# Optimization experiments

Measured on AMD Instinct MI355X. Metric: run time of the kernel, lower is better.

Reference implementation:

```python
import jax, jax.numpy as jnp
import numpy as np

TOKENS = 8192
HIDDEN = 6144
NUM_EXPERTS = 768  # n_routed_experts (512) + zero_expert_num (256)
TOP_K = 12
ROUTED_SCALING_FACTOR = 2.5


def setup_inputs() -> dict:
    key = jax.random.key(0)
    k1, k2, k3 = jax.random.split(key, 3)
    hidden_states = jax.random.normal(k1, (TOKENS, HIDDEN), dtype=jnp.float32)
    classifier_weight = jax.random.normal(k2, (NUM_EXPERTS, HIDDEN), dtype=jnp.float32) * (1.0 / np.sqrt(HIDDEN))
    e_score_correction_bias = jax.random.normal(k3, (NUM_EXPERTS,), dtype=jnp.float32) * 0.1
    return {
        "hidden_states": hidden_states,
        "classifier_weight": classifier_weight,
        "e_score_correction_bias": e_score_correction_bias,
    }


def reference(hidden_states, classifier_weight, e_score_correction_bias):
    # [T, H] -> router logits [T, E] in fp32 (source casts to float32)
    x = hidden_states.reshape(-1, HIDDEN).astype(jnp.float32)
    router_logits = jnp.einsum('th,eh->te', x, classifier_weight)

    # npu_moe_gating_top_k(renorm=0, norm_type=0): softmax scores,
    # bias-corrected selection, gather un-biased scores, scale.
    scores = jax.nn.softmax(router_logits, axis=-1)                # [T, E]
    scores_for_choice = scores + e_score_correction_bias[None, :]  # [T, E]
    _, topk_indices = jax.lax.top_k(scores_for_choice, TOP_K)       # [T, K]
    topk_weights = jnp.take_along_axis(scores, topk_indices, axis=-1)
    topk_weights = topk_weights * ROUTED_SCALING_FACTOR

    return topk_indices.astype(jnp.int32), topk_weights
```

## Files before the change

kernel.cpp:

```cpp
#include <hip/hip_runtime.h>

#define TOKENS  8192
#define HIDDEN  6144
#define EXPERTS 768
#define TOPK    12
#define RSF     2.5f
#define ROWH    (HIDDEN * 2)

typedef float    f4 __attribute__((ext_vector_type(4)));
typedef _Float16 h8 __attribute__((ext_vector_type(8)));
typedef _Float16 h2 __attribute__((ext_vector_type(2)));
typedef __fp16   g2 __attribute__((ext_vector_type(2)));

#define BM 128
#define BN 96
#define NKT 192
#define AH   8192
#define BLO  3072
#define BUFH 14336
#define LO_SCALE 4096.0f
#define LO_INV   2.44140625e-4f

static __device__ inline h2 pk(float a, float b) {
    g2 r = __builtin_amdgcn_cvt_pkrtz(a, b);
    return __builtin_bit_cast(h2, r);
}

static __device__ inline void cvt8(const f4 a, const f4 b, h8& hi, h8& lo) {
    h2 ha = pk(a.x, a.y), hb = pk(a.z, a.w), hc = pk(b.x, b.y), hd = pk(b.z, b.w);
    h2 la = pk((a.x - (float)ha[0]) * LO_SCALE, (a.y - (float)ha[1]) * LO_SCALE);
    h2 lb = pk((a.z - (float)hb[0]) * LO_SCALE, (a.w - (float)hb[1]) * LO_SCALE);
    h2 lc = pk((b.x - (float)hc[0]) * LO_SCALE, (b.y - (float)hc[1]) * LO_SCALE);
    h2 ld = pk((b.z - (float)hd[0]) * LO_SCALE, (b.w - (float)hd[1]) * LO_SCALE);
    hi[0]=ha[0]; hi[1]=ha[1]; hi[2]=hb[0]; hi[3]=hb[1];
    hi[4]=hc[0]; hi[5]=hc[1]; hi[6]=hd[0]; hi[7]=hd[1];
    lo[0]=la[0]; lo[1]=la[1]; lo[2]=lb[0]; lo[3]=lb[1];
    lo[4]=lc[0]; lo[5]=lc[1]; lo[6]=ld[0]; lo[7]=ld[1];
}

__global__ __launch_bounds__(256)
void split_convert_w(const float* W, _Float16* WO) {
    const int row = blockIdx.x;
    const float* src = W + (size_t)row * HIDDEN;
    _Float16*   dst = WO + (size_t)row * ROWH;
    const int t = threadIdx.x;
    f4 a[3], b[3];
#pragma unroll
    for (int i = 0; i < 3; ++i) {
        const f4* p = (const f4*)(src + (size_t)(t + 256 * i) * 8);
        a[i] = p[0]; b[i] = p[1];
    }
    __syncthreads();
#pragma unroll
    for (int i = 0; i < 3; ++i) {
        h8 hi, lo;
        cvt8(a[i], b[i], hi, lo);
        const int g = t + 256 * i;
        *(h8*)(dst + (size_t)g * 8)          = hi;
        *(h8*)(dst + HIDDEN + (size_t)g * 8) = lo;
    }
}

typedef __attribute__((address_space(1))) const void av1;
typedef __attribute__((address_space(3))) void av3;
static __device__ inline void stage16(const void* g, void* l) {
    __builtin_amdgcn_global_load_lds((av1*)g, (av3*)l, 16, 0, 0);
}

__global__ __launch_bounds__(256, 2)
void router_gemm(const float* __restrict__ X, const _Float16* __restrict__ Ws,
                 float* __restrict__ L) {
    __shared__ _Float16 sm[2 * BUFH];

    const int t    = threadIdx.x;
    const int bm   = blockIdx.x * BM;
    const int bn   = blockIdx.y * BN;
    const int lane = t & 63;
    const int w    = t >> 6;
    const int lr   = lane & 15;
    const int lq   = lane >> 4;

    const float* psA[4];
    uint32_t     ldsoA[4];
#pragma unroll
    for (int q = 0; q < 4; ++q) {
        const int jA = w * 4 + q;
        const int r  = jA * 8 + (lane >> 3);
        const int p  = lane & 7;
        const int c  = p ^ (r & 7);
        psA[q]   = X + (size_t)(bm + r) * HIDDEN + c * 4;
        ldsoA[q] = (uint32_t)(jA * 512);
    }

    const _Float16* psB[3];
    uint32_t        ldsoB[3];
#pragma unroll
    for (int q = 0; q < 3; ++q) {
        const int j    = w * 3 + q;
        const int isLo = (j >= 6);
        const int jj   = isLo ? j - 6 : j;
        const int r    = jj * 16 + (lane >> 2);
        const int p    = lane & 3;
        const int g    = p ^ ((r >> 1) & 3);
        psB[q]   = Ws + (size_t)(bn + r) * ROWH + g * 8 + isLo * HIDDEN;
        ldsoB[q] = (uint32_t)(AH + isLo * BLO + jj * 512);
    }

    uint32_t aoff[4];
#pragma unroll
    for (int mi = 0; mi < 4; ++mi) {
        const int r = (w & 1) * 64 + mi * 16 + lr;
        aoff[mi] = r * 64 + (uint32_t)(((2 * lq) ^ (r & 7)) * 8);
    }
    uint32_t boff[3];
#pragma unroll
    for (int ni = 0; ni < 3; ++ni) {
        const int r = (w >> 1) * 48 + ni * 16 + lr;
        boff[ni] = AH + r * 32 + ((lq ^ ((r >> 1) & 3)) * 8);
    }

    f4 acc_h[4][3], acc_c[4][3];
#pragma unroll
    for (int i = 0; i < 4; ++i)
#pragma unroll
        for (int j = 0; j < 3; ++j) { acc_h[i][j] = f4{0,0,0,0}; acc_c[i][j] = f4{0,0,0,0}; }

#pragma unroll
    for (int q = 0; q < 4; ++q) { stage16((const void*)psA[q], (void*)(sm + ldsoA[q])); psA[q] += 32; }
#pragma unroll
    for (int q = 0; q < 3; ++q) { stage16((const void*)psB[q], (void*)(sm + ldsoB[q])); psB[q] += 32; }

    auto do_tile = [&](const uint32_t boR, const uint32_t boW, const bool doStage) {
        if (doStage) {
#pragma unroll
            for (int q = 0; q < 4; ++q) { stage16((const void*)psA[q], (void*)(sm + boW + ldsoA[q])); psA[q] += 32; }
#pragma unroll
            for (int q = 0; q < 3; ++q) { stage16((const void*)psB[q], (void*)(sm + boW + ldsoB[q])); psB[q] += 32; }
        }
        h8 ah[4], al[4], bh[3], bl[3];
#pragma unroll
        for (int mi = 0; mi < 4; ++mi) {
            const uint32_t ao = boR + aoff[mi];
            const f4 va = *(const f4*)(sm + ao);
            const f4 vb = *(const f4*)(sm + (ao ^ 8u));
            cvt8(va, vb, ah[mi], al[mi]);
        }
#pragma unroll
        for (int ni = 0; ni < 3; ++ni) {
            bh[ni] = *(const h8*)(sm + boR + boff[ni]);
            bl[ni] = *(const h8*)(sm + boR + boff[ni] + BLO);
        }
#pragma unroll
        for (int mi = 0; mi < 4; ++mi)
#pragma unroll
            for (int ni = 0; ni < 3; ++ni) {
                acc_h[mi][ni] = __builtin_amdgcn_mfma_f32_16x16x32_f16(ah[mi], bh[ni], acc_h[mi][ni], 0, 0, 0);
                acc_c[mi][ni] = __builtin_amdgcn_mfma_f32_16x16x32_f16(ah[mi], bl[ni], acc_c[mi][ni], 0, 0, 0);
                acc_c[mi][ni] = __builtin_amdgcn_mfma_f32_16x16x32_f16(al[mi], bh[ni], acc_c[mi][ni], 0, 0, 0);
            }
    };

    for (int T2 = 0; T2 < NKT / 2; ++T2) {
        __syncthreads();
        do_tile(0u, (uint32_t)BUFH, true);
        __syncthreads();
        do_tile((uint32_t)BUFH, 0u, T2 != NKT / 2 - 1);
    }

#pragma unroll
    for (int mi = 0; mi < 4; ++mi)
#pragma unroll
        for (int ni = 0; ni < 3; ++ni)
#pragma unroll
            for (int r = 0; r < 4; ++r) {
                const int gm = bm + (w & 1) * 64 + mi * 16 + lq * 4 + r;
                const int gn = bn + (w >> 1) * 48 + ni * 16 + lr;
                L[(size_t)gm * EXPERTS + gn] = acc_h[mi][ni][r] + acc_c[mi][ni][r] * LO_INV;
            }
}

__global__ __launch_bounds__(256)
void router_topk(const float* __restrict__ L, const float* __restrict__ bias,
                 float* __restrict__ outIdx, float* __restrict__ outW) {
    __shared__ float sb[EXPERTS];
    const int t = threadIdx.x;
    for (int i = t; i < EXPERTS; i += 256) sb[i] = bias[i];
    __syncthreads();

    const int lane  = t & 63;
    const int wave  = t >> 6;
    const int token = blockIdx.x * 4 + wave;
    const float* row = L + (size_t)token * EXPERTS;

    float lg[12];
#pragma unroll
    for (int j = 0; j < 12; ++j) lg[j] = row[lane + 64 * j];

    float m = lg[0];
#pragma unroll
    for (int j = 1; j < 12; ++j) m = fmaxf(m, lg[j]);
#pragma unroll
    for (int o = 32; o > 0; o >>= 1) m = fmaxf(m, __shfl_xor(m, o));

    float s = 0.0f;
#pragma unroll
    for (int j = 0; j < 12; ++j) { lg[j] = __expf(lg[j] - m); s += lg[j]; }
#pragma unroll
    for (int o = 32; o > 0; o >>= 1) s += __shfl_xor(s, o);
    const float inv = 1.0f / s;

    float cand[12];
#pragma unroll
    for (int j = 0; j < 12; ++j) {
        lg[j] *= inv;
        cand[j] = lg[j] + sb[lane + 64 * j];
    }

#pragma unroll
    for (int r = 0; r < TOPK; ++r) {
        float bv = -__builtin_inff();
        int   bi = EXPERTS;
#pragma unroll
        for (int j = 0; j < 12; ++j) {
            const int e = lane + 64 * j;
            const bool better = (cand[j] > bv) || (cand[j] == bv && e < bi);
            bv = better ? cand[j] : bv;
            bi = better ? e : bi;
        }
#pragma unroll
        for (int o = 32; o > 0; o >>= 1) {
            const float ov = __shfl_xor(bv, o);
            const int   oi = __shfl_xor(bi, o);
            const bool better = (ov > bv) || (ov == bv && oi < bi);
            bv = better ? ov : bv;
            bi = better ? oi : bi;
        }
        if (lane == 0) {
            outIdx[token * TOPK + r] = (float)bi;
            outW  [token * TOPK + r] = (bv - sb[bi]) * RSF;
        }
        if ((bi & 63) == lane) {
            const int slot = bi >> 6;
#pragma unroll
            for (int j = 0; j < 12; ++j)
                if (j == slot) cand[j] = -__builtin_inff();
        }
    }
}

extern "C" void kernel_launch(void* const* d_in, const int* in_sizes, int n_in,
                              void* d_out, int out_size, void* d_ws, size_t ws_size,
                              hipStream_t stream) {
    float* X = (float*)d_in[0];
    float* W = (float*)d_in[1];
    const float* B = (const float*)d_in[2];

    const size_t bytesW = (size_t)EXPERTS * HIDDEN * sizeof(float);
    const size_t bytesL = (size_t)TOKENS * EXPERTS * sizeof(float);

    _Float16* Ws; float* logits;
    if (ws_size >= bytesW + bytesL) {
        char* p = (char*)d_ws;
        Ws     = (_Float16*)p;
        logits = (float*)(p + bytesW);
    } else {
        Ws     = (_Float16*)W;
        logits = (float*)d_ws;
    }

    float* outIdx = (float*)d_out;
    float* outW   = outIdx + (size_t)TOKENS * TOPK;

    split_convert_w<<<EXPERTS, 256, 0, stream>>>(W, Ws);

    dim3 grid_gemm(TOKENS / BM, EXPERTS / BN);
    router_gemm<<<grid_gemm, 256, 0, stream>>>((const float*)X, (const _Float16*)Ws, logits);
    router_topk<<<TOKENS / 4, 256, 0, stream>>>(logits, B, outIdx, outW);
}
```

Baseline: 507.3 us.

## Convert X tile to fp16 hi/lo at staging time instead of per-read

```diff
diff --git a/kernel.cpp b/kernel.cpp
--- a/kernel.cpp
+++ b/kernel.cpp
@@ -9,15 +9,17 @@
 
 typedef float    f4 __attribute__((ext_vector_type(4)));
 typedef _Float16 h8 __attribute__((ext_vector_type(8)));
+typedef _Float16 h4 __attribute__((ext_vector_type(4)));
 typedef _Float16 h2 __attribute__((ext_vector_type(2)));
 typedef __fp16   g2 __attribute__((ext_vector_type(2)));
 
 #define BM 128
 #define BN 96
 #define NKT 192
-#define AH   8192
-#define BLO  3072
-#define BUFH 14336
+#define AHALF 4096
+#define AH    8192
+#define BLO   3072
+#define BUFH  14336
 #define LO_SCALE 4096.0f
 #define LO_INV   2.44140625e-4f
 
@@ -26,16 +28,21 @@
     return __builtin_bit_cast(h2, r);
 }
 
+static __device__ inline void cvt4(const f4 a, h4& hi, h4& lo) {
+    h2 h01 = pk(a.x, a.y), h23 = pk(a.z, a.w);
+    h2 l01 = pk((a.x - (float)h01[0]) * LO_SCALE, (a.y - (float)h01[1]) * LO_SCALE);
+    h2 l23 = pk((a.z - (float)h23[0]) * LO_SCALE, (a.w - (float)h23[1]) * LO_SCALE);
+    hi[0]=h01[0]; hi[1]=h01[1]; hi[2]=h23[0]; hi[3]=h23[1];
+    lo[0]=l01[0]; lo[1]=l01[1]; lo[2]=l23[0]; lo[3]=l23[1];
+}
+
 static __device__ inline void cvt8(const f4 a, const f4 b, h8& hi, h8& lo) {
-    h2 ha = pk(a.x, a.y), hb = pk(a.z, a.w), hc = pk(b.x, b.y), hd = pk(b.z, b.w);
-    h2 la = pk((a.x - (float)ha[0]) * LO_SCALE, (a.y - (float)ha[1]) * LO_SCALE);
-    h2 lb = pk((a.z - (float)hb[0]) * LO_SCALE, (a.w - (float)hb[1]) * LO_SCALE);
-    h2 lc = pk((b.x - (float)hc[0]) * LO_SCALE, (b.y - (float)hc[1]) * LO_SCALE);
-    h2 ld = pk((b.z - (float)hd[0]) * LO_SCALE, (b.w - (float)hd[1]) * LO_SCALE);
-    hi[0]=ha[0]; hi[1]=ha[1]; hi[2]=hb[0]; hi[3]=hb[1];
-    hi[4]=hc[0]; hi[5]=hc[1]; hi[6]=hd[0]; hi[7]=hd[1];
-    lo[0]=la[0]; lo[1]=la[1]; lo[2]=lb[0]; lo[3]=lb[1];
-    lo[4]=lc[0]; lo[5]=lc[1]; lo[6]=ld[0]; lo[7]=ld[1];
+    h4 ha, la, hb, lb;
+    cvt4(a, ha, la); cvt4(b, hb, lb);
+    hi[0]=ha[0]; hi[1]=ha[1]; hi[2]=ha[2]; hi[3]=ha[3];
+    hi[4]=hb[0]; hi[5]=hb[1]; hi[6]=hb[2]; hi[7]=hb[3];
+    lo[0]=la[0]; lo[1]=la[1]; lo[2]=la[2]; lo[3]=la[3];
+    lo[4]=lb[0]; lo[5]=lb[1]; lo[6]=lb[2]; lo[7]=lb[3];
 }
 
 __global__ __launch_bounds__(256)
@@ -81,15 +88,14 @@
     const int lq   = lane >> 4;
 
     const float* psA[4];
-    uint32_t     ldsoA[4];
+    uint32_t     wofA[4];
 #pragma unroll
     for (int q = 0; q < 4; ++q) {
         const int jA = w * 4 + q;
         const int r  = jA * 8 + (lane >> 3);
-        const int p  = lane & 7;
-        const int c  = p ^ (r & 7);
-        psA[q]   = X + (size_t)(bm + r) * HIDDEN + c * 4;
-        ldsoA[q] = (uint32_t)(jA * 512);
+        const int c  = lane & 7;
+        psA[q]  = X + (size_t)(bm + r) * HIDDEN + c * 4;
+        wofA[q] = (uint32_t)(r * 32 + (((c >> 1) ^ ((r >> 1) & 3)) * 8) + (c & 1) * 4);
     }
 
     const _Float16* psB[3];
@@ -110,13 +116,13 @@
 #pragma unroll
     for (int mi = 0; mi < 4; ++mi) {
         const int r = (w & 1) * 64 + mi * 16 + lr;
-        aoff[mi] = r * 64 + (uint32_t)(((2 * lq) ^ (r & 7)) * 8);
+        aoff[mi] = (uint32_t)(r * 32 + ((lq ^ ((r >> 1) & 3)) * 8));
     }
     uint32_t boff[3];
 #pragma unroll
     for (int ni = 0; ni < 3; ++ni) {
         const int r = (w >> 1) * 48 + ni * 16 + lr;
-        boff[ni] = AH + r * 32 + ((lq ^ ((r >> 1) & 3)) * 8);
+        boff[ni] = (uint32_t)(AH + r * 32 + ((lq ^ ((r >> 1) & 3)) * 8));
     }
 
     f4 acc_h[4][3], acc_c[4][3];
@@ -126,24 +132,28 @@
         for (int j = 0; j < 3; ++j) { acc_h[i][j] = f4{0,0,0,0}; acc_c[i][j] = f4{0,0,0,0}; }
 
 #pragma unroll
-    for (int q = 0; q < 4; ++q) { stage16((const void*)psA[q], (void*)(sm + ldsoA[q])); psA[q] += 32; }
+    for (int q = 0; q < 4; ++q) {
+        f4 av = *(const f4*)psA[q]; psA[q] += 32;
+        h4 hi, lo; cvt4(av, hi, lo);
+        *(h4*)(sm + wofA[q])         = hi;
+        *(h4*)(sm + wofA[q] + AHALF) = lo;
+    }
 #pragma unroll
     for (int q = 0; q < 3; ++q) { stage16((const void*)psB[q], (void*)(sm + ldsoB[q])); psB[q] += 32; }
 
     auto do_tile = [&](const uint32_t boR, const uint32_t boW, const bool doStage) {
+        f4 av[4];
         if (doStage) {
 #pragma unroll
-            for (int q = 0; q < 4; ++q) { stage16((const void*)psA[q], (void*)(sm + boW + ldsoA[q])); psA[q] += 32; }
+            for (int q = 0; q < 4; ++q) { av[q] = *(const f4*)psA[q]; psA[q] += 32; }
 #pragma unroll
             for (int q = 0; q < 3; ++q) { stage16((const void*)psB[q], (void*)(sm + boW + ldsoB[q])); psB[q] += 32; }
         }
         h8 ah[4], al[4], bh[3], bl[3];
 #pragma unroll
         for (int mi = 0; mi < 4; ++mi) {
-            const uint32_t ao = boR + aoff[mi];
-            const f4 va = *(const f4*)(sm + ao);
-            const f4 vb = *(const f4*)(sm + (ao ^ 8u));
-            cvt8(va, vb, ah[mi], al[mi]);
+            ah[mi] = *(const h8*)(sm + boR + aoff[mi]);
+            al[mi] = *(const h8*)(sm + boR + aoff[mi] + AHALF);
         }
 #pragma unroll
         for (int ni = 0; ni < 3; ++ni) {
@@ -158,6 +168,14 @@
                 acc_c[mi][ni] = __builtin_amdgcn_mfma_f32_16x16x32_f16(ah[mi], bl[ni], acc_c[mi][ni], 0, 0, 0);
                 acc_c[mi][ni] = __builtin_amdgcn_mfma_f32_16x16x32_f16(al[mi], bh[ni], acc_c[mi][ni], 0, 0, 0);
             }
+        if (doStage) {
+#pragma unroll
+            for (int q = 0; q < 4; ++q) {
+                h4 hi, lo; cvt4(av[q], hi, lo);
+                *(h4*)(sm + boW + wofA[q])         = hi;
+                *(h4*)(sm + boW + wofA[q] + AHALF) = lo;
+            }
+        }
     };
 
     for (int T2 = 0; T2 < NKT / 2; ++T2) {
```

After: 535.0 us. +5.5%, slower.
